# Optimization experiments

Hardware: AMD Instinct MI355X
Metric: run time of the kernel (lower is better)

## Reference

```python
import jax, jax.numpy as jnp
import numpy as np

DIM = 256; HEADS = 8; HD = DIM // HEADS; WIN = 3; LOCAL = WIN * WIN
SR = 8; SHARED = 4; ROUTED = 2
B = 4; RES = 64; TBL = 4096
EPS = 1.1920929e-07  # torch.finfo(float32).eps


def _l2(x):
    return x / jnp.clip(jnp.linalg.norm(x, axis=-1, keepdims=True), EPS)


def _forward(x, relative_coords_table, q_w, q_b, kv_w, kv_b, temperature,
             query_embedding, rpb_local, learnable_tokens, learnable_bias,
             cpb1_w, cpb1_b, cpb2_w, cpb2_b, sr_w, sr_b, norm_g, norm_b,
             wg_w, wg0_w, wg1_w, proj_w, proj_b, relative_pos_index, H, W):
    B_, N, C = x.shape
    pH, pW = H // SR, W // SR
    PL = pH * pW
    _x = x.reshape(B_ * N, C)

    # ---- MoE head routing: top-k gating over routed heads ----
    gates = jax.nn.softmax(_x @ wg_w.T, axis=1)                 # (BN, n_routed)
    _, idx = jax.lax.top_k(gates, ROUTED)
    mask = jax.nn.one_hot(idx, gates.shape[1], dtype=gates.dtype).sum(axis=1)
    rg = gates * mask
    rg = rg / jnp.clip(jnp.sum(rg, axis=1, keepdims=True), EPS)
    routed_gates = rg.reshape(B_, N, -1) * ROUTED

    # ---- seq-length-scale buffer: log(local valid-window count + pool_len) ----
    r = WIN // 2
    ch = np.minimum(np.arange(H) + r, H - 1) - np.maximum(np.arange(H) - r, 0) + 1
    cw = np.minimum(np.arange(W) + r, W - 1) - np.maximum(np.arange(W) - r, 0) + 1
    sls = jnp.asarray(np.log(np.outer(ch, cw).reshape(-1, 1).astype(np.float32) + PL))

    # ---- queries ----
    q = (x @ q_w.T + q_b).reshape(B_, N, HEADS, HD).transpose(0, 2, 1, 3)
    q_norm = _l2(q)                                             # (B,h,N,d)
    q_scaled = (q_norm + query_embedding) * jax.nn.softplus(temperature) * sls

    # ---- local branch: unfold normalized k and v over 3x3 windows (zero pad) ----
    kv = x @ kv_w.T + kv_b                                      # (B,N,2C)
    k_loc = _l2(kv[..., :C].reshape(B_, N, HEADS, HD)).reshape(B_, N, C)
    kvl = jnp.concatenate([k_loc, kv[..., C:]], -1).transpose(0, 2, 1).reshape(B_, 2 * C, H, W)
    kvp = jnp.pad(kvl, ((0, 0), (0, 0), (r, r), (r, r)))
    patches = jnp.stack([kvp[:, :, i:i + H, j:j + W] for i in range(WIN) for j in range(WIN)], axis=2)
    patches = patches.reshape(B_, 2 * HEADS, HD, LOCAL, N).transpose(0, 1, 4, 2, 3)  # (B,2h,N,d,L)
    k_local, v_local = patches[:, :HEADS], patches[:, HEADS:]

    attn_local = jnp.einsum('bhnd,bhndl->bhnl', q_scaled, k_local) + rpb_local[:, None, :]

    # ---- pooled global branch ----
    x_ = x.transpose(0, 2, 1).reshape(B_, C, H, W)
    x_ = jnp.einsum('oc,bchw->bohw', sr_w, x_) + sr_b[None, :, None, None]  # 1x1 conv
    x_ = jax.nn.gelu(x_, approximate=False)
    x_ = x_.reshape(B_, C, pH, SR, pW, SR).mean((3, 5)).reshape(B_, C, PL).transpose(0, 2, 1)
    mu = x_.mean(-1, keepdims=True)
    var = ((x_ - mu) ** 2).mean(-1, keepdims=True)
    x_ = (x_ - mu) / jnp.sqrt(var + 1e-5) * norm_g + norm_b
    kvp2 = (x_ @ kv_w.T + kv_b).reshape(B_, PL, 2 * HEADS, HD).transpose(0, 2, 1, 3)
    k_pool, v_pool = kvp2[:, :HEADS], kvp2[:, HEADS:]

    cpb = jax.nn.relu(relative_coords_table @ cpb1_w.T + cpb1_b) @ cpb2_w.T + cpb2_b  # (T,h)
    pool_bias = cpb.T[:, relative_pos_index.reshape(-1)].reshape(HEADS, N, PL)
    attn_pool = jnp.einsum('bhnd,bhpd->bhnp', q_scaled, _l2(k_pool)) + pool_bias

    # ---- joint softmax over local + pooled keys ----
    attn = jax.nn.softmax(jnp.concatenate([attn_local, attn_pool], axis=-1), axis=-1)
    a_loc, a_pool = attn[..., :LOCAL], attn[..., LOCAL:]
    a_loc = jnp.einsum('bhnd,hdl->bhnl', q_norm, learnable_tokens) + learnable_bias + a_loc
    x_local = jnp.einsum('bhnl,bhndl->bhnd', a_loc, v_local)
    x_pool = jnp.einsum('bhnp,bhpd->bhnd', a_pool, v_pool)
    out = (x_local + x_pool).transpose(0, 2, 1, 3)              # (B,N,h,d)

    # ---- combine shared + routed head gates ----
    shared_gates = jax.nn.softmax(_x @ wg1_w.T, axis=1).reshape(B_, N, SHARED) * SHARED
    w0 = jax.nn.softmax(_x @ wg0_w.T, axis=1).reshape(B_, N, 2) * 2
    masked = jnp.concatenate([w0[..., 0:1] * shared_gates, w0[..., 1:2] * routed_gates], axis=-1)
    out = (masked[..., None] * out).reshape(B_, N, C)
    return out @ proj_w.T + proj_b


def setup_inputs() -> dict:
    key = jax.random.key(0)
    ks = jax.random.split(key, 20)
    H = W = RES
    N = H * W
    C = DIM
    PL = (H // SR) * (W // SR)

    def nrm(i, shape, s=0.02):
        return jax.random.normal(ks[i], shape, dtype=jnp.float32) * s

    return {
        'x': jax.random.normal(ks[0], (B, N, C), dtype=jnp.float32),
        'relative_coords_table': jax.random.normal(ks[1], (TBL, 2), dtype=jnp.float32),
        'q_w': nrm(3, (C, C)), 'q_b': jnp.zeros((C,), jnp.float32),
        'kv_w': nrm(4, (2 * C, C)), 'kv_b': jnp.zeros((2 * C,), jnp.float32),
        'temperature': jnp.full((HEADS, 1, 1), float(np.log(np.exp(1 / 0.24) - 1)), jnp.float32),
        'query_embedding': nrm(5, (HEADS, 1, HD)),
        'rpb_local': nrm(6, (HEADS, LOCAL), 0.0004),
        'learnable_tokens': nrm(7, (HEADS, HD, LOCAL)),
        'learnable_bias': jnp.zeros((HEADS, 1, LOCAL), jnp.float32),
        'cpb1_w': nrm(8, (512, 2)), 'cpb1_b': jnp.zeros((512,), jnp.float32),
        'cpb2_w': nrm(9, (HEADS, 512)), 'cpb2_b': jnp.zeros((HEADS,), jnp.float32),
        'sr_w': nrm(10, (C, C)), 'sr_b': jnp.zeros((C,), jnp.float32),
        'norm_g': jnp.ones((C,), jnp.float32), 'norm_b': jnp.zeros((C,), jnp.float32),
        'wg_w': nrm(11, (HEADS - SHARED, C)),
        'wg0_w': nrm(12, (2, C)),
        'wg1_w': nrm(13, (SHARED, C)),
        'proj_w': nrm(14, (C, C)), 'proj_b': jnp.zeros((C,), jnp.float32),
        'relative_pos_index': jax.random.randint(ks[2], (N, PL), 0, TBL, dtype=jnp.int32),
        'H': H, 'W': W,
    }


def reference(x, relative_coords_table, q_w, q_b, kv_w, kv_b, temperature,
              query_embedding, rpb_local, learnable_tokens, learnable_bias,
              cpb1_w, cpb1_b, cpb2_w, cpb2_b, sr_w, sr_b, norm_g, norm_b,
              wg_w, wg0_w, wg1_w, proj_w, proj_b, relative_pos_index, H, W):
    return _forward(x, relative_coords_table, q_w, q_b, kv_w, kv_b, temperature,
                    query_embedding, rpb_local, learnable_tokens, learnable_bias,
                    cpb1_w, cpb1_b, cpb2_w, cpb2_b, sr_w, sr_b, norm_g, norm_b,
                    wg_w, wg0_w, wg1_w, proj_w, proj_b, relative_pos_index, H, W)
```

## Files before the change

### kernel.cpp

```cpp
#include <hip/hip_runtime.h>
#include <math.h>

#define EPSF 1.1920929e-07f

typedef __attribute__((ext_vector_type(8))) short short8;
typedef __attribute__((ext_vector_type(4))) float f32x4;

static __device__ __forceinline__ unsigned short f2bf(float f) {
    unsigned int u = __float_as_uint(f);
    return (unsigned short)((u + 0x7FFFu + ((u >> 16) & 1u)) >> 16);
}
static __device__ __forceinline__ float bf2f(unsigned short u) {
    return __uint_as_float((unsigned int)u << 16);
}

__global__ __launch_bounds__(256) void prep_kernel(
    const float* __restrict__ x,
    const float* __restrict__ wg,  const float* __restrict__ wg0,
    const float* __restrict__ wg1,
    const float* __restrict__ q_w, const float* __restrict__ kv_w,
    const float* __restrict__ sr_w, const float* __restrict__ pw,
    const float* __restrict__ tbl,
    const float* __restrict__ c1w, const float* __restrict__ c1b,
    const float* __restrict__ c2w, const float* __restrict__ c2b,
    unsigned short* __restrict__ xbf, float* __restrict__ gate,
    unsigned short* __restrict__ wcat, unsigned short* __restrict__ pwbf,
    float* __restrict__ kv_wT, float* __restrict__ cpb)
{
    __shared__ float shpad[512];
    const int blk = blockIdx.x;
    const int t   = threadIdx.x;
    if (blk < 4096) {
        const int j = t & 63;
        const int row = (blk << 2) + (t >> 6);
        float4 v = *(const float4*)(x + (size_t)row*256 + j*4);
        ushort4 o;
        o.x = f2bf(v.x); o.y = f2bf(v.y); o.z = f2bf(v.z); o.w = f2bf(v.w);
        *(ushort4*)(xbf + (size_t)row*256 + j*4) = o;
        float d[10];
#pragma unroll
        for (int f = 0; f < 10; ++f) {
            const float* wf = (f < 4) ? (wg + f*256) : (f < 6) ? (wg0 + (f-4)*256)
                                                               : (wg1 + (f-6)*256);
            float4 wv = *(const float4*)(wf + j*4);
            float s = v.x*wv.x + v.y*wv.y + v.z*wv.z + v.w*wv.w;
            s += __shfl_xor(s, 32); s += __shfl_xor(s, 16); s += __shfl_xor(s, 8);
            s += __shfl_xor(s, 4);  s += __shfl_xor(s, 2);  s += __shfl_xor(s, 1);
            d[f] = s;
        }
        if (j == 0) {
            float e[4];
            float m = fmaxf(fmaxf(d[0],d[1]), fmaxf(d[2],d[3]));
            float ssum = 0.f;
            for (int i = 0; i < 4; ++i) { e[i] = expf(d[i]-m); ssum += e[i]; }
            for (int i = 0; i < 4; ++i) e[i] /= ssum;
            int i1 = 0;
            for (int i = 1; i < 4; ++i) if (e[i] > e[i1]) i1 = i;
            int i2 = -1;
            for (int i = 0; i < 4; ++i) if (i != i1 && (i2 < 0 || e[i] > e[i2])) i2 = i;
            float rs = fmaxf(e[i1] + e[i2], EPSF);
            float rg[4] = {0.f,0.f,0.f,0.f};
            rg[i1] = e[i1] / rs * 2.f;
            rg[i2] = e[i2] / rs * 2.f;
            float sh[4];
            float m1 = fmaxf(fmaxf(d[6],d[7]), fmaxf(d[8],d[9]));
            float s1 = 0.f;
            for (int i = 0; i < 4; ++i) { sh[i] = expf(d[6+i]-m1); s1 += sh[i]; }
            float mm = fmaxf(d[4], d[5]);
            float e0 = expf(d[4]-mm), e1 = expf(d[5]-mm);
            float w00 = e0/(e0+e1)*2.f, w01 = e1/(e0+e1)*2.f;
            float* gr = gate + ((size_t)row << 3);
            for (int i = 0; i < 4; ++i) gr[i]   = w00 * (sh[i]/s1*4.f);
            for (int i = 0; i < 4; ++i) gr[4+i] = w01 * rg[i];
        }
    } else if (blk < 4416) {
        const int e = ((blk - 4096)*256 + t)*4;
        if (e < 262144) {
            int n = e >> 8, k = e & 255;
            const float* src = (n < 256) ? (q_w + n*256) :
                               (n < 768) ? (kv_w + (n-256)*256) : (sr_w + (n-768)*256);
            float4 v = *(const float4*)(src + k);
            ushort4 o;
            o.x = f2bf(v.x); o.y = f2bf(v.y); o.z = f2bf(v.z); o.w = f2bf(v.w);
            *(ushort4*)(wcat + e) = o;
        } else {
            int e2 = e - 262144;
            float4 v = *(const float4*)(pw + e2);
            ushort4 o;
            o.x = f2bf(v.x); o.y = f2bf(v.y); o.z = f2bf(v.z); o.w = f2bf(v.w);
            *(ushort4*)(pwbf + e2) = o;
        }
    } else if (blk < 4544) {
        const int e = ((blk - 4416)*256 + t)*4;
        int o = e >> 8, k = e & 255;
        float4 v = *(const float4*)(kv_w + e);
        kv_wT[(k+0)*512 + o] = v.x;
        kv_wT[(k+1)*512 + o] = v.y;
        kv_wT[(k+2)*512 + o] = v.z;
        kv_wT[(k+3)*512 + o] = v.w;
    } else {
        const int r = blk - 4544;
        const float c0 = tbl[(size_t)r*2], c1 = tbl[(size_t)r*2+1];
        for (int i = t; i < 512; i += 256)
            shpad[i] = fmaxf(c0*c1w[i*2] + c1*c1w[i*2+1] + c1b[i], 0.f);
        __syncthreads();
        const int hh = t >> 5, dd = t & 31;
        float s = 0.f;
        for (int i = dd; i < 512; i += 32) s += shpad[i] * c2w[hh*512+i];
        for (int off = 16; off; off >>= 1) s += __shfl_xor(s, off, 32);
        if (dd == 0) cpb[(size_t)hh*4096 + r] = (s + c2b[hh]) * 1.44269504089f;
    }
}

__global__ __launch_bounds__(256) void gemm_mfma(
    const unsigned short* __restrict__ A,
    const unsigned short* __restrict__ W,
    const float* __restrict__ B0, const float* __restrict__ B1,
    const float* __restrict__ B2,
    int r1, int r2, int mode,
    float* __restrict__ C, int ldc,
    unsigned short* __restrict__ qkv,
    const float* __restrict__ temp, const float* __restrict__ qe)
{
    __shared__ __attribute__((aligned(16))) unsigned short Bt[64*264];
    const int m0 = blockIdx.y << 6;
    const int n0 = blockIdx.x << 6;
    const int t  = threadIdx.x;
    const int w  = t >> 6;
    const int col16 = t & 15;
    const int quad  = (t & 63) >> 4;

    const float* Bp; int noff;
    if (n0 < r1)      { Bp = B0; noff = 0;  }
    else if (n0 < r2) { Bp = B1; noff = r1; }
    else              { Bp = B2; noff = r2; }

    short8 afr[8];
    {
        const unsigned short* ap = A + (size_t)(m0 + w*16 + col16)*256 + quad*8;
#pragma unroll
        for (int kk = 0; kk < 8; ++kk)
            afr[kk] = *(const short8*)(ap + kk*32);
    }
#pragma unroll
    for (int j = 0; j < 8; ++j) {
        int ci = j*256 + t;
        int r = ci >> 5, c = ci & 31;
        uint4 bv = *(const uint4*)(W + (size_t)(n0 + r)*256 + c*8);
        *(uint4*)(Bt + r*264 + c*8) = bv;
    }
    __syncthreads();

    f32x4 acc[4];
#pragma unroll
    for (int ct = 0; ct < 4; ++ct) acc[ct] = (f32x4){0.f, 0.f, 0.f, 0.f};
#pragma unroll
    for (int kk = 0; kk < 8; ++kk) {
#pragma unroll
        for (int ct = 0; ct < 4; ++ct) {
            short8 bf = *(const short8*)(Bt + (ct*16 + col16)*264 + kk*32 + quad*8);
            acc[ct] = __builtin_amdgcn_mfma_f32_16x16x32_bf16(afr[kk], bf, acc[ct], 0, 0, 0);
        }
    }

    float bias_c[4];
#pragma unroll
    for (int ct = 0; ct < 4; ++ct)
        bias_c[ct] = Bp[n0 + ct*16 + col16 - noff];

    if (mode == 0) {
        const int region = n0 >> 8;
        float qe_c[4], spt_c[4];
        if (region == 0) {
#pragma unroll
            for (int c = 0; c < 4; ++c) {
                int col = n0 + c*16 + col16;
                spt_c[c] = log1pf(expf(temp[(col >> 5) & 7])) * 1.44269504089f;
                qe_c[c]  = qe[col];
            }
        }
#pragma unroll
        for (int reg = 0; reg < 4; ++reg) {
            const int row = m0 + w*16 + quad*4 + reg;
            float v[4];
#pragma unroll
            for (int c = 0; c < 4; ++c) v[c] = acc[c][reg] + bias_c[c];
            if (region <= 1) {
#pragma unroll
                for (int hp = 0; hp < 2; ++hp) {
                    float s = v[2*hp]*v[2*hp] + v[2*hp+1]*v[2*hp+1];
                    s += __shfl_xor(s, 1); s += __shfl_xor(s, 2);
                    s += __shfl_xor(s, 4); s += __shfl_xor(s, 8);
                    float inv = 1.0f / fmaxf(sqrtf(s), EPSF);
                    v[2*hp]   *= inv;
                    v[2*hp+1] *= inv;
                }
            }
            if (region == 0) {
                int n = row & 4095;
                int y = n >> 6, x = n & 63;
                int cy = (y == 0 || y == 63) ? 2 : 3;
                int cx = (x == 0 || x == 63) ? 2 : 3;
                float sls = logf((float)(cy*cx) + 64.0f);
#pragma unroll
                for (int c = 0; c < 4; ++c)
                    v[c] = (v[c] + qe_c[c]) * (spt_c[c] * sls);
            }
            if (region == 3) {
#pragma unroll
                for (int c = 0; c < 4; ++c) {
                    float g = 0.5f * v[c] * (1.0f + erff(v[c] * 0.70710678118654752f));
                    C[(size_t)row * ldc + n0 + c*16 + col16] = g;
                }
            } else {
#pragma unroll
                for (int c = 0; c < 4; ++c)
                    qkv[(size_t)row * 2048 + n0 + c*16 + col16] = f2bf(v[c]);
            }
        }
    } else {
#pragma unroll
        for (int reg = 0; reg < 4; ++reg) {
            const int row = m0 + w*16 + quad*4 + reg;
#pragma unroll
            for (int c = 0; c < 4; ++c)
                C[(size_t)row * ldc + n0 + c*16 + col16] = acc[c][reg] + bias_c[c];
        }
    }
}

__global__ __launch_bounds__(256) void poolkv_kernel(
    const float* __restrict__ buf,
    const float* __restrict__ g, const float* __restrict__ bb,
    const float* __restrict__ kv_wT, const float* __restrict__ kv_b,
    unsigned short* __restrict__ kpb, unsigned short* __restrict__ vpb)
{
    __shared__ float r1[256], r2[256];
    __shared__ float xs[256];
    __shared__ float rowv[512];
    __shared__ float inv[8];
    const int blk = blockIdx.x;
    const int b = blk >> 6, p = blk & 63;
    const int py = p >> 3, px = p & 7;
    const int t = threadIdx.x;
    float acc = 0.f;
    for (int dy = 0; dy < 8; ++dy)
#pragma unroll
        for (int dx = 0; dx < 8; ++dx) {
            int s = ((py*8+dy) << 6) + px*8 + dx;
            acc += buf[(((size_t)(b*4096+s)) << 10) + 768 + t];
        }
    acc *= (1.0f/64.0f);
    r1[t] = acc; r2[t] = acc*acc;
    __syncthreads();
    for (int off = 128; off; off >>= 1) {
        if (t < off) { r1[t] += r1[t+off]; r2[t] += r2[t+off]; }
        __syncthreads();
    }
    float mu  = r1[0] * (1.0f/256.0f);
    float var = r2[0] * (1.0f/256.0f) - mu*mu;
    float rstd = rsqrtf(var + 1e-5f);
    xs[t] = (acc - mu) * rstd * g[t] + bb[t];
    __syncthreads();
    {
        float s0 = kv_b[t], s1 = kv_b[256 + t];
#pragma unroll 4
        for (int k = 0; k < 256; ++k) {
            float xv = xs[k];
            const float* wr = kv_wT + (size_t)k*512;
            s0 += xv * wr[t];
            s1 += xv * wr[256 + t];
        }
        rowv[t] = s0; rowv[256 + t] = s1;
    }
    __syncthreads();
    if (t < 8) {
        float s = 0.f;
        for (int dd = 0; dd < 32; ++dd) { float v = rowv[t*32+dd]; s += v*v; }
        inv[t] = 1.0f / fmaxf(sqrtf(s), EPSF);
    }
    __syncthreads();
    const int h  = t >> 5;
    const int dd = t & 31;
    size_t ob = (size_t)(b*8+h) << 11;
    kpb[ob + ((size_t)p << 5) + dd] = f2bf(rowv[t] * inv[h]);
    vpb[ob + ((size_t)dd << 6) + p] = f2bf(rowv[256 + t]);
}

__global__ __launch_bounds__(256, 5) void attn_mfma(
    const unsigned short* __restrict__ qkv,
    unsigned short* __restrict__ ao,
    const unsigned short* __restrict__ kpb,
    const unsigned short* __restrict__ vpb,
    const float* __restrict__ cpb,
    const int*   __restrict__ rpi,
    const float* __restrict__ temp,
    const float* __restrict__ qe,
    const float* __restrict__ rpb,
    const float* __restrict__ lt,
    const float* __restrict__ lb,
    const float* __restrict__ gate)
{
    __shared__ __attribute__((aligned(16))) unsigned char SMEM[32624];
    unsigned short* U0  = (unsigned short*)SMEM;
    unsigned short* U1  = (unsigned short*)(SMEM + 8960);
    unsigned short* P   = (unsigned short*)(SMEM + 14080);
    unsigned short* LTT = (unsigned short*)(SMEM + 31488);
    float* dqvL = (float*)(SMEM + 32512);
    float* rpbL = (float*)(SMEM + 32576);
    float* cpbL = (float*)P;

    const int tile = blockIdx.x;
    const int h    = blockIdx.y;
    const int b    = blockIdx.z;
    const int ty0  = (tile >> 3) << 3;
    const int tx0  = (tile & 7) << 3;
    const int t    = threadIdx.x;
    const int lane  = t & 63;
    const int w     = t >> 6;
    const int col16 = lane & 15;
    const int quad  = lane >> 4;
    const int s_w   = (20*w) & ~15;

    const int nq = w*16 + col16;
    const int qy = ty0 + (nq >> 3), qx = tx0 + (nq & 7);
    short8 aq = *(const short8*)(qkv +
        ((size_t)(b*4096 + ((qy<<6)|qx)))*2048 + h*32 + quad*8);

    int rpv[4][4];
#pragma unroll
    for (int ct = 0; ct < 4; ++ct) {
        int p = ct*16 + col16;
#pragma unroll
        for (int reg = 0; reg < 4; ++reg) {
            int n = w*16 + quad*4 + reg;
            int y = ty0 + (n >> 3), x = tx0 + (n & 7);
            rpv[ct][reg] = rpi[(size_t)((y << 6) | x)*64 + p];
        }
    }

    for (int i = t; i < 896; i += 256) {
        int r = i >> 3, sg = i & 7;
        uint2 val = {0u, 0u};
        if (r < 100) {
            int y = ty0 + r/10 - 1, x = tx0 + r%10 - 1;
            if (y >= 0 && y < 64 && x >= 0 && x < 64)
                val = *(const uint2*)(qkv +
                    (size_t)(b*4096 + ((y<<6)|x))*2048 + h*32 + 256 + sg*4);
        }
        *(uint2*)(U0 + r*40 + sg*4) = val;
    }
    {
        const unsigned short* src = kpb + (size_t)(b*8+h)*2048;
        for (int i = t; i < 512; i += 256)
            *(uint2*)(U1 + (i >> 3)*40 + (i & 7)*4) = *(const uint2*)(src + i*4);
    }
    const float spt  = log1pf(expf(temp[h]));
    const float sptL = spt * 1.44269504089f;
    if (t >= 64 && t < 80) {
        int j = t - 64;
        float s = 0.f;
        if (j < 9) {
            s = lb[h*9 + j];
            for (int dd = 0; dd < 32; ++dd)
                s -= qe[h*32+dd] * lt[(h*32+dd)*9 + j];
        }
        dqvL[j] = s;
    } else if (t >= 80 && t < 89) {
        rpbL[t-80] = rpb[h*9 + (t-80)] * 1.44269504089f;
    }
    for (int i = t; i < 512; i += 256) {
        int j = i >> 5, dd = i & 31;
        LTT[j*32 + dd] = (j < 9) ? f2bf(lt[(h*32+dd)*9 + j]) : (unsigned short)0;
    }
    {
        const float4* src = (const float4*)(cpb + (size_t)h*4096);
        float4* dst = (float4*)cpbL;
        for (int i = t; i < 1024; i += 256) dst[i] = src[i];
    }
    __syncthreads();

    float pbias[4][4];
#pragma unroll
    for (int ct = 0; ct < 4; ++ct)
#pragma unroll
        for (int reg = 0; reg < 4; ++reg)
            pbias[ct][reg] = cpbL[rpv[ct][reg]];

    f32x4 cl[4], cp[4];
    {
        const f32x4 z = {0.f, 0.f, 0.f, 0.f};
#pragma unroll
        for (int ct = 0; ct < 4; ++ct) {
            short8 bk = *(const short8*)(U0 + (s_w + ct*16 + col16)*40 + quad*8);
            cl[ct] = __builtin_amdgcn_mfma_f32_16x16x32_bf16(aq, bk, z, 0, 0, 0);
        }
#pragma unroll
        for (int ct = 0; ct < 4; ++ct) {
            short8 bp = *(const short8*)(U1 + (ct*16 + col16)*40 + quad*8);
            cp[ct] = __builtin_amdgcn_mfma_f32_16x16x32_bf16(aq, bp, z, 0, 0, 0);
        }
    }
#pragma unroll
    for (int ct = 0; ct < 4; ++ct) {
        int hk = s_w + ct*16 + col16;
        int ky = hk / 10, kx = hk - ky*10;
#pragma unroll
        for (int reg = 0; reg < 4; ++reg) {
            int n = w*16 + quad*4 + reg;
            int dy = ky - (n >> 3), dx = kx - (n & 7);
            bool valid = (dy >= 0 && dy <= 2 && dx >= 0 && dx <= 2);
            cl[ct][reg] = valid ? (cl[ct][reg] + rpbL[dy*3 + dx]) : -1e30f;
        }
    }
#pragma unroll
    for (int ct = 0; ct < 4; ++ct)
#pragma unroll
        for (int reg = 0; reg < 4; ++reg)
            cp[ct][reg] += pbias[ct][reg];

    __syncthreads();

    float inv[4];
#pragma unroll
    for (int reg = 0; reg < 4; ++reg) {
        float m = -1e30f;
#pragma unroll
        for (int ct = 0; ct < 4; ++ct) m = fmaxf(m, cl[ct][reg]);
#pragma unroll
        for (int ct = 0; ct < 4; ++ct) m = fmaxf(m, cp[ct][reg]);
        m = fmaxf(m, __shfl_xor(m, 1)); m = fmaxf(m, __shfl_xor(m, 2));
        m = fmaxf(m, __shfl_xor(m, 4)); m = fmaxf(m, __shfl_xor(m, 8));
        float s = 0.f;
#pragma unroll
        for (int ct = 0; ct < 4; ++ct) {
            float e = exp2f(cl[ct][reg] - m); cl[ct][reg] = e; s += e;
        }
#pragma unroll
        for (int ct = 0; ct < 4; ++ct) {
            float e = exp2f(cp[ct][reg] - m); cp[ct][reg] = e; s += e;
        }
        s += __shfl_xor(s, 1); s += __shfl_xor(s, 2);
        s += __shfl_xor(s, 4); s += __shfl_xor(s, 8);
        inv[reg] = 1.0f / s;
    }
#pragma unroll
    for (int ct = 0; ct < 4; ++ct)
#pragma unroll
        for (int reg = 0; reg < 4; ++reg) {
            int n = w*16 + quad*4 + reg;
            P[n*136 + ct*16 + col16] = f2bf(cl[ct][reg] * inv[reg]);
        }
#pragma unroll
    for (int ct = 0; ct < 4; ++ct)
#pragma unroll
        for (int reg = 0; reg < 4; ++reg) {
            int n = w*16 + quad*4 + reg;
            P[n*136 + 64 + ct*16 + col16] = f2bf(cp[ct][reg] * inv[reg]);
        }
    {
        const f32x4 z = {0.f, 0.f, 0.f, 0.f};
        short8 blt = *(const short8*)(LTT + col16*32 + quad*8);
        f32x4 cd = __builtin_amdgcn_mfma_f32_16x16x32_bf16(aq, blt, z, 0, 0, 0);
        if (col16 < 9) {
            const float iA = 1.0f / (sptL * 4.2195077052f);
            const float iB = 1.0f / (sptL * 4.2484952420f);
            const float iC = 1.0f / (sptL * 4.2904594411f);
            int dy = col16 / 3, dx = col16 - dy*3;
#pragma unroll
            for (int reg = 0; reg < 4; ++reg) {
                int n = w*16 + quad*4 + reg;
                int y = ty0 + (n >> 3), x = tx0 + (n & 7);
                int cs = ((y==0||y==63)?2:3) + ((x==0||x==63)?2:3);
                float isc = (cs == 4) ? iA : (cs == 5) ? iB : iC;
                float ltv = cd[reg] * isc + dqvL[col16];
                int hk = ((n >> 3) + dy)*10 + (n & 7) + dx;
                int pc = hk - s_w;
                P[n*136 + pc] = f2bf(bf2f(P[n*136 + pc]) + ltv);
            }
        }
    }
    __syncthreads();

    float gv[4];
#pragma unroll
    for (int reg = 0; reg < 4; ++reg) {
        int n = w*16 + quad*4 + reg;
        int y = ty0 + (n >> 3), x = tx0 + (n & 7);
        gv[reg] = gate[(((size_t)(b*4096 + ((y<<6)|x))) << 3) + h];
    }
    unsigned short* VT  = U0;
    unsigned short* VPT = U1;
    for (int i = t; i < 896; i += 256) {
        int r = i >> 3, sg = i & 7;
        uint2 val = {0u, 0u};
        if (r < 100) {
            int y = ty0 + r/10 - 1, x = tx0 + r%10 - 1;
            if (y >= 0 && y < 64 && x >= 0 && x < 64)
                val = *(const uint2*)(qkv +
                    (size_t)(b*4096 + ((y<<6)|x))*2048 + h*32 + 512 + sg*4);
        }
        int d0 = sg << 2;
        VT[(d0+0)*136 + r] = (unsigned short)(val.x & 0xffffu);
        VT[(d0+1)*136 + r] = (unsigned short)(val.x >> 16);
        VT[(d0+2)*136 + r] = (unsigned short)(val.y & 0xffffu);
        VT[(d0+3)*136 + r] = (unsigned short)(val.y >> 16);
    }
    {
        const unsigned short* vsrc = vpb + (size_t)(b*8+h)*2048;
        for (int i = t; i < 512; i += 256) {
            int d = i >> 4, p4 = (i & 15) << 2;
            *(uint2*)(VPT + d*72 + p4) = *(const uint2*)(vsrc + d*64 + p4);
        }
    }
    __syncthreads();

    f32x4 o0 = {0.f,0.f,0.f,0.f}, o1 = {0.f,0.f,0.f,0.f};
#pragma unroll
    for (int ks = 0; ks < 4; ++ks) {
        short8 a = *(const short8*)(P + (w*16 + col16)*136 + ks*32 + quad*8);
        short8 b0, b1;
        if (ks < 2) {
            b0 = *(const short8*)(VT + col16*136      + s_w + ks*32 + quad*8);
            b1 = *(const short8*)(VT + (16+col16)*136 + s_w + ks*32 + quad*8);
        } else {
            b0 = *(const short8*)(VPT + col16*72      + (ks-2)*32 + quad*8);
            b1 = *(const short8*)(VPT + (16+col16)*72 + (ks-2)*32 + quad*8);
        }
        o0 = __builtin_amdgcn_mfma_f32_16x16x32_bf16(a, b0, o0, 0, 0, 0);
        o1 = __builtin_amdgcn_mfma_f32_16x16x32_bf16(a, b1, o1, 0, 0, 0);
    }
#pragma unroll
    for (int reg = 0; reg < 4; ++reg) {
        int n = w*16 + quad*4 + reg;
        int y = ty0 + (n >> 3), x = tx0 + (n & 7);
        size_t rowo = (size_t)(b*4096 + ((y<<6)|x))*256 + h*32;
        float g = gv[reg];
        ao[rowo + col16]      = f2bf(o0[reg] * g);
        ao[rowo + 16 + col16] = f2bf(o1[reg] * g);
    }
}

extern "C" void kernel_launch(void* const* d_in, const int* in_sizes, int n_in,
                              void* d_out, int out_size, void* d_ws, size_t ws_size,
                              hipStream_t stream)
{
    const float* x    = (const float*)d_in[0];
    const float* tbl  = (const float*)d_in[1];
    const float* q_w  = (const float*)d_in[2];
    const float* q_b  = (const float*)d_in[3];
    const float* kv_w = (const float*)d_in[4];
    const float* kv_b = (const float*)d_in[5];
    const float* temp = (const float*)d_in[6];
    const float* qe   = (const float*)d_in[7];
    const float* rpb  = (const float*)d_in[8];
    const float* lt   = (const float*)d_in[9];
    const float* lb   = (const float*)d_in[10];
    const float* c1w  = (const float*)d_in[11];
    const float* c1b  = (const float*)d_in[12];
    const float* c2w  = (const float*)d_in[13];
    const float* c2b  = (const float*)d_in[14];
    const float* sr_w = (const float*)d_in[15];
    const float* sr_b = (const float*)d_in[16];
    const float* ng   = (const float*)d_in[17];
    const float* nbias= (const float*)d_in[18];
    const float* wg   = (const float*)d_in[19];
    const float* wg0  = (const float*)d_in[20];
    const float* wg1  = (const float*)d_in[21];
    const float* pw   = (const float*)d_in[22];
    const float* pb   = (const float*)d_in[23];
    const int*   rpi  = (const int*)d_in[24];
    (void)in_sizes; (void)n_in; (void)out_size; (void)ws_size;

    float* buf   = (float*)d_ws;
    unsigned short* qkvb = (unsigned short*)d_ws;
    float* xp    = buf + (size_t)16384*1024;
    float* kpoolf= xp + 65536;
    unsigned short* kpb = (unsigned short*)kpoolf;
    unsigned short* vpb = kpb + 131072;
    float* cpbb  = kpoolf + 131072;
    float* gateb = cpbb + 32768;
    float* kvwT  = gateb + 131072;
    unsigned short* xbf  = (unsigned short*)(kvwT + 131072);
    unsigned short* ao   = xbf;
    unsigned short* wcat = xbf + (size_t)16384*256;
    unsigned short* pwbf = wcat + 262144;
    float* out   = (float*)d_out;

    prep_kernel<<<8640,256,0,stream>>>(x, wg, wg0, wg1, q_w, kv_w, sr_w, pw,
                                       tbl, c1w, c1b, c2w, c2b,
                                       xbf, gateb, wcat, pwbf, kvwT, cpbb);
    gemm_mfma<<<dim3(16,256),256,0,stream>>>(xbf, wcat, q_b, kv_b, sr_b,
                                             256, 768, 0, buf, 1024,
                                             qkvb, temp, qe);
    poolkv_kernel<<<256,256,0,stream>>>(buf, ng, nbias, kvwT, kv_b, kpb, vpb);
    attn_mfma<<<dim3(64,8,4),256,0,stream>>>(qkvb, ao, kpb, vpb, cpbb, rpi,
                                             temp, qe, rpb, lt, lb, gateb);
    gemm_mfma<<<dim3(4,256),256,0,stream>>>(ao, pwbf, pb, pb, pb,
                                            1<<30, 1<<30, 1, out, 256,
                                            (unsigned short*)nullptr, nullptr, nullptr);
}
```

Before: 225.4 us.

## Reuse GEMM weight tile across two row blocks and split pooled-KV projection

```diff
diff --git a/kernel.cpp b/kernel.cpp
--- a/kernel.cpp
+++ b/kernel.cpp
@@ -123,10 +123,10 @@
     const float* __restrict__ temp, const float* __restrict__ qe)
 {
     __shared__ __attribute__((aligned(16))) unsigned short Bt[64*264];
-    const int m0 = blockIdx.y << 6;
-    const int n0 = blockIdx.x << 6;
-    const int t  = threadIdx.x;
-    const int w  = t >> 6;
+    const int m0b = blockIdx.y << 7;
+    const int n0  = blockIdx.x << 6;
+    const int t   = threadIdx.x;
+    const int w   = t >> 6;
     const int col16 = t & 15;
     const int quad  = (t & 63) >> 4;
 
@@ -135,12 +135,12 @@
     else if (n0 < r2) { Bp = B1; noff = r1; }
     else              { Bp = B2; noff = r2; }
 
-    short8 afr[8];
+    short8 afrA[8];
     {
-        const unsigned short* ap = A + (size_t)(m0 + w*16 + col16)*256 + quad*8;
+        const unsigned short* ap = A + (size_t)(m0b + w*16 + col16)*256 + quad*8;
 #pragma unroll
         for (int kk = 0; kk < 8; ++kk)
-            afr[kk] = *(const short8*)(ap + kk*32);
+            afrA[kk] = *(const short8*)(ap + kk*32);
     }
 #pragma unroll
     for (int j = 0; j < 8; ++j) {
@@ -151,6 +151,75 @@
     }
     __syncthreads();
 
+    float bias_c[4];
+#pragma unroll
+    for (int ct = 0; ct < 4; ++ct)
+        bias_c[ct] = Bp[n0 + ct*16 + col16 - noff];
+
+    const int region = n0 >> 8;
+    float qe_c[4], spt_c[4];
+    if (mode == 0 && region == 0) {
+#pragma unroll
+        for (int c = 0; c < 4; ++c) {
+            int col = n0 + c*16 + col16;
+            spt_c[c] = log1pf(expf(temp[(col >> 5) & 7])) * 1.44269504089f;
+            qe_c[c]  = qe[col];
+        }
+    }
+
+    auto epilogue = [&](f32x4* acc, int m0) {
+        if (mode == 0) {
+#pragma unroll
+            for (int reg = 0; reg < 4; ++reg) {
+                const int row = m0 + w*16 + quad*4 + reg;
+                float v[4];
+#pragma unroll
+                for (int c = 0; c < 4; ++c) v[c] = acc[c][reg] + bias_c[c];
+                if (region <= 1) {
+#pragma unroll
+                    for (int hp = 0; hp < 2; ++hp) {
+                        float s = v[2*hp]*v[2*hp] + v[2*hp+1]*v[2*hp+1];
+                        s += __shfl_xor(s, 1); s += __shfl_xor(s, 2);
+                        s += __shfl_xor(s, 4); s += __shfl_xor(s, 8);
+                        float inv = 1.0f / fmaxf(sqrtf(s), EPSF);
+                        v[2*hp]   *= inv;
+                        v[2*hp+1] *= inv;
+                    }
+                }
+                if (region == 0) {
+                    int n = row & 4095;
+                    int y = n >> 6, x = n & 63;
+                    int cs = ((y==0||y==63)?2:3) + ((x==0||x==63)?2:3);
+                    float sls = (cs == 4) ? 4.2195077052f :
+                                (cs == 5) ? 4.2484952420f :
+                                            4.2904594411f;
+#pragma unroll
+                    for (int c = 0; c < 4; ++c)
+                        v[c] = (v[c] + qe_c[c]) * (spt_c[c] * sls);
+                }
+                if (region == 3) {
+#pragma unroll
+                    for (int c = 0; c < 4; ++c) {
+                        float g = 0.5f * v[c] * (1.0f + erff(v[c] * 0.70710678118654752f));
+                        C[(size_t)row * ldc + n0 + c*16 + col16] = g;
+                    }
+                } else {
+#pragma unroll
+                    for (int c = 0; c < 4; ++c)
+                        qkv[(size_t)row * 2048 + n0 + c*16 + col16] = f2bf(v[c]);
+                }
+            }
+        } else {
+#pragma unroll
+            for (int reg = 0; reg < 4; ++reg) {
+                const int row = m0 + w*16 + quad*4 + reg;
+#pragma unroll
+                for (int c = 0; c < 4; ++c)
+                    C[(size_t)row * ldc + n0 + c*16 + col16] = acc[c][reg] + bias_c[c];
+            }
+        }
+    };
+
     f32x4 acc[4];
 #pragma unroll
     for (int ct = 0; ct < 4; ++ct) acc[ct] = (f32x4){0.f, 0.f, 0.f, 0.f};
@@ -159,74 +228,29 @@
 #pragma unroll
         for (int ct = 0; ct < 4; ++ct) {
             short8 bf = *(const short8*)(Bt + (ct*16 + col16)*264 + kk*32 + quad*8);
-            acc[ct] = __builtin_amdgcn_mfma_f32_16x16x32_bf16(afr[kk], bf, acc[ct], 0, 0, 0);
-        }
-    }
-
-    float bias_c[4];
-#pragma unroll
-    for (int ct = 0; ct < 4; ++ct)
-        bias_c[ct] = Bp[n0 + ct*16 + col16 - noff];
-
-    if (mode == 0) {
-        const int region = n0 >> 8;
-        float qe_c[4], spt_c[4];
-        if (region == 0) {
-#pragma unroll
-            for (int c = 0; c < 4; ++c) {
-                int col = n0 + c*16 + col16;
-                spt_c[c] = log1pf(expf(temp[(col >> 5) & 7])) * 1.44269504089f;
-                qe_c[c]  = qe[col];
-            }
-        }
-#pragma unroll
-        for (int reg = 0; reg < 4; ++reg) {
-            const int row = m0 + w*16 + quad*4 + reg;
-            float v[4];
-#pragma unroll
-            for (int c = 0; c < 4; ++c) v[c] = acc[c][reg] + bias_c[c];
-            if (region <= 1) {
-#pragma unroll
-                for (int hp = 0; hp < 2; ++hp) {
-                    float s = v[2*hp]*v[2*hp] + v[2*hp+1]*v[2*hp+1];
-                    s += __shfl_xor(s, 1); s += __shfl_xor(s, 2);
-                    s += __shfl_xor(s, 4); s += __shfl_xor(s, 8);
-                    float inv = 1.0f / fmaxf(sqrtf(s), EPSF);
-                    v[2*hp]   *= inv;
-                    v[2*hp+1] *= inv;
-                }
-            }
-            if (region == 0) {
-                int n = row & 4095;
-                int y = n >> 6, x = n & 63;
-                int cy = (y == 0 || y == 63) ? 2 : 3;
-                int cx = (x == 0 || x == 63) ? 2 : 3;
-                float sls = logf((float)(cy*cx) + 64.0f);
-#pragma unroll
-                for (int c = 0; c < 4; ++c)
-                    v[c] = (v[c] + qe_c[c]) * (spt_c[c] * sls);
-            }
-            if (region == 3) {
-#pragma unroll
-                for (int c = 0; c < 4; ++c) {
-                    float g = 0.5f * v[c] * (1.0f + erff(v[c] * 0.70710678118654752f));
-                    C[(size_t)row * ldc + n0 + c*16 + col16] = g;
-                }
-            } else {
-#pragma unroll
-                for (int c = 0; c < 4; ++c)
-                    qkv[(size_t)row * 2048 + n0 + c*16 + col16] = f2bf(v[c]);
-            }
-        }
-    } else {
-#pragma unroll
-        for (int reg = 0; reg < 4; ++reg) {
-            const int row = m0 + w*16 + quad*4 + reg;
-#pragma unroll
-            for (int c = 0; c < 4; ++c)
-                C[(size_t)row * ldc + n0 + c*16 + col16] = acc[c][reg] + bias_c[c];
-        }
-    }
+            acc[ct] = __builtin_amdgcn_mfma_f32_16x16x32_bf16(afrA[kk], bf, acc[ct], 0, 0, 0);
+        }
+    }
+    short8 afrB[8];
+    {
+        const unsigned short* ap = A + (size_t)(m0b + 64 + w*16 + col16)*256 + quad*8;
+#pragma unroll
+        for (int kk = 0; kk < 8; ++kk)
+            afrB[kk] = *(const short8*)(ap + kk*32);
+    }
+    epilogue(acc, m0b);
+
+#pragma unroll
+    for (int ct = 0; ct < 4; ++ct) acc[ct] = (f32x4){0.f, 0.f, 0.f, 0.f};
+#pragma unroll
+    for (int kk = 0; kk < 8; ++kk) {
+#pragma unroll
+        for (int ct = 0; ct < 4; ++ct) {
+            short8 bf = *(const short8*)(Bt + (ct*16 + col16)*264 + kk*32 + quad*8);
+            acc[ct] = __builtin_amdgcn_mfma_f32_16x16x32_bf16(afrB[kk], bf, acc[ct], 0, 0, 0);
+        }
+    }
+    epilogue(acc, m0b + 64);
 }
 
 __global__ __launch_bounds__(256) void poolkv_kernel(
@@ -235,15 +259,18 @@
     const float* __restrict__ kv_wT, const float* __restrict__ kv_b,
     unsigned short* __restrict__ kpb, unsigned short* __restrict__ vpb)
 {
-    __shared__ float r1[256], r2[256];
     __shared__ float xs[256];
-    __shared__ float rowv[512];
-    __shared__ float inv[8];
-    const int blk = blockIdx.x;
-    const int b = blk >> 6, p = blk & 63;
+    __shared__ float red[8];
+    const int blk  = blockIdx.x;
+    const int half = blk & 1;
+    const int bp   = blk >> 1;
+    const int b = bp >> 6, p = bp & 63;
     const int py = p >> 3, px = p & 7;
     const int t = threadIdx.x;
+    const int lane = t & 63, w = t >> 6;
+
     float acc = 0.f;
+#pragma unroll
     for (int dy = 0; dy < 8; ++dy)
 #pragma unroll
         for (int dx = 0; dx < 8; ++dx) {
@@ -251,40 +278,40 @@
             acc += buf[(((size_t)(b*4096+s)) << 10) + 768 + t];
         }
     acc *= (1.0f/64.0f);
-    r1[t] = acc; r2[t] = acc*acc;
+
+    float a1 = acc, a2 = acc*acc;
+    a1 += __shfl_xor(a1, 32); a2 += __shfl_xor(a2, 32);
+    a1 += __shfl_xor(a1, 16); a2 += __shfl_xor(a2, 16);
+    a1 += __shfl_xor(a1, 8);  a2 += __shfl_xor(a2, 8);
+    a1 += __shfl_xor(a1, 4);  a2 += __shfl_xor(a2, 4);
+    a1 += __shfl_xor(a1, 2);  a2 += __shfl_xor(a2, 2);
+    a1 += __shfl_xor(a1, 1);  a2 += __shfl_xor(a2, 1);
+    if (lane == 0) { red[w] = a1; red[4 + w] = a2; }
     __syncthreads();
-    for (int off = 128; off; off >>= 1) {
-        if (t < off) { r1[t] += r1[t+off]; r2[t] += r2[t+off]; }
-        __syncthreads();
-    }
-    float mu  = r1[0] * (1.0f/256.0f);
-    float var = r2[0] * (1.0f/256.0f) - mu*mu;
-    float rstd = rsqrtf(var + 1e-5f);
+    float mu = (red[0]+red[1]+red[2]+red[3]) * (1.0f/256.0f);
+    float ms = (red[4]+red[5]+red[6]+red[7]) * (1.0f/256.0f);
+    float rstd = rsqrtf(ms - mu*mu + 1e-5f);
     xs[t] = (acc - mu) * rstd * g[t] + bb[t];
     __syncthreads();
-    {
-        float s0 = kv_b[t], s1 = kv_b[256 + t];
-#pragma unroll 4
-        for (int k = 0; k < 256; ++k) {
-            float xv = xs[k];
-            const float* wr = kv_wT + (size_t)k*512;
-            s0 += xv * wr[t];
-            s1 += xv * wr[256 + t];
-        }
-        rowv[t] = s0; rowv[256 + t] = s1;
-    }
-    __syncthreads();
-    if (t < 8) {
-        float s = 0.f;
-        for (int dd = 0; dd < 32; ++dd) { float v = rowv[t*32+dd]; s += v*v; }
-        inv[t] = 1.0f / fmaxf(sqrtf(s), EPSF);
-    }
-    __syncthreads();
-    const int h  = t >> 5;
-    const int dd = t & 31;
-    size_t ob = (size_t)(b*8+h) << 11;
-    kpb[ob + ((size_t)p << 5) + dd] = f2bf(rowv[t] * inv[h]);
-    vpb[ob + ((size_t)dd << 6) + p] = f2bf(rowv[256 + t]);
+
+    float s = kv_b[half*256 + t];
+    const float* wbase = kv_wT + half*256 + t;
+#pragma unroll 8
+    for (int k = 0; k < 256; ++k)
+        s += xs[k] * wbase[(size_t)k*512];
+
+    const int h = t >> 5, dd = t & 31;
+    const size_t ob = (size_t)(b*8+h) << 11;
+    if (half == 0) {
+        float s2 = s*s;
+        s2 += __shfl_xor(s2, 1); s2 += __shfl_xor(s2, 2);
+        s2 += __shfl_xor(s2, 4); s2 += __shfl_xor(s2, 8);
+        s2 += __shfl_xor(s2, 16);
+        float invn = 1.0f / fmaxf(sqrtf(s2), EPSF);
+        kpb[ob + ((size_t)p << 5) + dd] = f2bf(s * invn);
+    } else {
+        vpb[ob + ((size_t)dd << 6) + p] = f2bf(s);
+    }
 }
 
 __global__ __launch_bounds__(256, 5) void attn_mfma(
@@ -590,13 +617,13 @@
     prep_kernel<<<8640,256,0,stream>>>(x, wg, wg0, wg1, q_w, kv_w, sr_w, pw,
                                        tbl, c1w, c1b, c2w, c2b,
                                        xbf, gateb, wcat, pwbf, kvwT, cpbb);
-    gemm_mfma<<<dim3(16,256),256,0,stream>>>(xbf, wcat, q_b, kv_b, sr_b,
+    gemm_mfma<<<dim3(16,128),256,0,stream>>>(xbf, wcat, q_b, kv_b, sr_b,
                                              256, 768, 0, buf, 1024,
                                              qkvb, temp, qe);
-    poolkv_kernel<<<256,256,0,stream>>>(buf, ng, nbias, kvwT, kv_b, kpb, vpb);
+    poolkv_kernel<<<512,256,0,stream>>>(buf, ng, nbias, kvwT, kv_b, kpb, vpb);
     attn_mfma<<<dim3(64,8,4),256,0,stream>>>(qkvb, ao, kpb, vpb, cpbb, rpi,
                                              temp, qe, rpb, lt, lb, gateb);
-    gemm_mfma<<<dim3(4,256),256,0,stream>>>(ao, pwbf, pb, pb, pb,
+    gemm_mfma<<<dim3(4,128),256,0,stream>>>(ao, pwbf, pb, pb, pb,
                                             1<<30, 1<<30, 1, out, 256,
                                             (unsigned short*)nullptr, nullptr, nullptr);
 }
```

Result: no change. 222.3 us (-1.4%).
